# Kernel tuning notes

Measured on AMD Instinct MI355X. Metric: run time of the kernel, lower is better.

Reference implementation:

```python
import jax, jax.numpy as jnp
import numpy as np

B, H, W, C = 32, 64, 64, 192
WS, SS, NH = 8, 4, 6
N = WS * WS            # tokens per window = 64
n1, n2 = H // WS, W // WS
nW = n1 * n2           # windows per image = 64
Dh = C // NH           # head dim = 32
SCALE = Dh ** -0.5


def _rel_pos_index():
    coords = np.stack(np.meshgrid(np.arange(WS), np.arange(WS), indexing='ij')).reshape(2, -1)
    rel = (coords[:, :, None] - coords[:, None, :]).transpose(1, 2, 0)
    rel[:, :, 0] += WS - 1
    rel[:, :, 1] += WS - 1
    rel[:, :, 0] *= 2 * WS - 1
    return rel.sum(-1)  # (N, N) int


def _attn_mask():
    img = np.zeros((H, W))
    slices = (slice(0, -WS), slice(-WS, -SS), slice(-SS, None))
    cnt = 0
    for hs in slices:
        for ws in slices:
            img[hs, ws] = cnt
            cnt += 1
    mw = img.reshape(n1, WS, n2, WS).transpose(0, 2, 1, 3).reshape(nW, N)
    am = mw[:, None, :] - mw[:, :, None]  # (nW, N, N)
    return np.where(am != 0, -100.0, 0.0).astype(np.float32)


RPI = jnp.asarray(_rel_pos_index().reshape(-1))  # (N*N,) constant index
MASK = jnp.asarray(_attn_mask())                  # (nW, N, N) constant


def setup_inputs() -> dict:
    key = jax.random.key(0)
    ks = jax.random.split(key, 6)
    r = lambda k, s: jax.random.normal(k, s, jnp.float32) * 0.02
    return {
        'x': jax.random.normal(ks[0], (B, H * W, C), jnp.float32),
        'norm1_g': jnp.ones((C,), jnp.float32), 'norm1_b': jnp.zeros((C,), jnp.float32),
        'qkv_w': r(ks[1], (C, 3 * C)), 'qkv_b': jnp.zeros((3 * C,), jnp.float32),
        'proj_w': r(ks[2], (C, C)), 'proj_b': jnp.zeros((C,), jnp.float32),
        'rpb': r(ks[3], ((2 * WS - 1) ** 2, NH)),
        'norm2_g': jnp.ones((C,), jnp.float32), 'norm2_b': jnp.zeros((C,), jnp.float32),
        'fc1_w': r(ks[4], (C, 4 * C)), 'fc1_b': jnp.zeros((4 * C,), jnp.float32),
        'fc2_w': r(ks[5], (4 * C, C)), 'fc2_b': jnp.zeros((C,), jnp.float32),
    }


def _ln(x, g, b):
    m = jnp.mean(x, axis=-1, keepdims=True)
    v = jnp.mean(jnp.square(x - m), axis=-1, keepdims=True)
    return (x - m) * jax.lax.rsqrt(v + 1e-5) * g + b


def reference(x, norm1_g, norm1_b, qkv_w, qkv_b, proj_w, proj_b, rpb,
              norm2_g, norm2_b, fc1_w, fc1_b, fc2_w, fc2_b):
    shortcut = x
    h = _ln(x, norm1_g, norm1_b).reshape(B, H, W, C)
    h = jnp.roll(h, (-SS, -SS), axis=(1, 2))  # cyclic shift
    # window partition: (B, H, W, C) -> (B*nW, N, C), batch-major window order
    h = h.reshape(B, n1, WS, n2, WS, C).transpose(0, 1, 3, 2, 4, 5).reshape(B * nW, N, C)
    qkv = (h @ qkv_w + qkv_b).reshape(B * nW, N, 3, NH, Dh)
    q = qkv[:, :, 0].transpose(0, 2, 1, 3)  # (Bw, NH, N, Dh)
    k = qkv[:, :, 1].transpose(0, 2, 1, 3)
    v = qkv[:, :, 2].transpose(0, 2, 1, 3)
    scores = jnp.einsum('bhid,bhjd->bhij', q, k) * SCALE
    bias = rpb[RPI].reshape(N, N, NH).transpose(2, 0, 1)  # (NH, N, N)
    scores = scores + bias[None]
    # faithful to source: flat window axis reinterpreted as (num_w, B) for masking
    scores = (scores.reshape(nW, B, NH, N, N) + MASK[:, None, None]).reshape(B * nW, NH, N, N)
    probs = jax.nn.softmax(scores, axis=-1)
    ctx = jnp.einsum('bhij,bhjd->bhid', probs, v).transpose(0, 2, 1, 3).reshape(B * nW, N, C)
    ctx = ctx @ proj_w + proj_b
    # window reverse + un-shift
    h = ctx.reshape(B, n1, n2, WS, WS, C).transpose(0, 1, 3, 2, 4, 5).reshape(B, H, W, C)
    h = jnp.roll(h, (SS, SS), axis=(1, 2)).reshape(B, H * W, C)
    x = shortcut + h
    y = _ln(x, norm2_g, norm2_b)
    y = jax.nn.gelu(y @ fc1_w + fc1_b, approximate=False)
    return x + (y @ fc2_w + fc2_b)
```

## Files before the change

### kernel.cpp

```cpp
#include <hip/hip_runtime.h>
#include <hip/hip_bf16.h>


#define DI __device__ __forceinline__

typedef __attribute__((ext_vector_type(8))) short bhalf8;
typedef __attribute__((ext_vector_type(4))) float f32x4;
typedef unsigned short u16;
typedef unsigned int   u32;

DI u32 f2bf2(float a, float b){
  u32 r;
  asm("v_cvt_pk_bf16_f32 %0, %1, %2" : "=v"(r) : "v"(a), "v"(b));
  return r;
}
DI u16 f2bf(float f){ return (u16)f2bf2(f, f); }

DI float fast_gelu(float x){
  float s = __expf(-1.702f * x);
  return x * __builtin_amdgcn_rcpf(1.0f + s);
}

DI int tok2glob(int t){
  int n = t & 63, widx = t >> 6;
  int b = widx >> 6, wi = widx & 63;
  int hh = ((wi >> 3) << 3) + (n >> 3);
  int ww = ((wi & 7) << 3) + (n & 7);
  int hs = (hh + 4) & 63, wsv = (ww + 4) & 63;
  return (b << 12) + (hs << 6) + wsv;
}

DI int region_id(int hpos, int wpos){
  int rh = (hpos < 56) ? 0 : ((hpos < 60) ? 1 : 2);
  int rw = (wpos < 56) ? 0 : ((wpos < 60) ? 1 : 2);
  return rh*3 + rw;
}

__global__ void transcast_kernel(const float* __restrict__ W, u16* __restrict__ Wt, int K, int N){
  int idx = blockIdx.x * 256 + threadIdx.x;
  if (idx < K*N){
    int n = idx / K, k = idx - n*K;
    Wt[idx] = f2bf(W[(size_t)k * N + n]);
  }
}

__global__ __launch_bounds__(768, 3) void attn_fused_kernel(
    const float* __restrict__ x, const float* __restrict__ n1g, const float* __restrict__ n1b,
    const u16* __restrict__ qkvWt, const float* __restrict__ qkv_b,
    const u16* __restrict__ projWt, const float* __restrict__ proj_b,
    float* __restrict__ out, const float* __restrict__ rpb){
  __shared__ u16 AsB[64*192];
  __shared__ u16 QKB[64*384];
  __shared__ u16 Vt[6][32*64];
  __shared__ float Rlds[225*6];
  int widx = blockIdx.x;
  int tid  = threadIdx.x;
  int w = tid >> 6, lane = tid & 63, lr = lane & 15, lg = lane >> 4;

  if (w >= 8){
    for (int i = tid - 512; i < 225*6; i += 256) Rlds[i] = rpb[i];
  } else {
    int qrow = tid >> 3, oct = tid & 7;
    int g = tok2glob(widx*64 + qrow);
    const float4* xr = (const float4*)(x + (size_t)g*192 + oct*24);
    float4 va[6];
    float s = 0.f, sq = 0.f;
    #pragma unroll
    for (int j = 0; j < 6; j++){
      va[j] = xr[j];
      s  += va[j].x + va[j].y + va[j].z + va[j].w;
      sq += va[j].x*va[j].x + va[j].y*va[j].y + va[j].z*va[j].z + va[j].w*va[j].w;
    }
    s  += __shfl_xor(s, 1, 64);  sq += __shfl_xor(sq, 1, 64);
    s  += __shfl_xor(s, 2, 64);  sq += __shfl_xor(sq, 2, 64);
    s  += __shfl_xor(s, 4, 64);  sq += __shfl_xor(sq, 4, 64);
    float mean = s * (1.f/192.f);
    float rstd = rsqrtf(sq * (1.f/192.f) - mean*mean + 1e-5f);
    const float4* g4 = (const float4*)(n1g + oct*24);
    const float4* b4 = (const float4*)(n1b + oct*24);
    #pragma unroll
    for (int j2 = 0; j2 < 3; j2++){
      float4 v0 = va[2*j2], v1 = va[2*j2+1];
      float4 g0 = g4[2*j2], g1 = g4[2*j2+1];
      float4 b0 = b4[2*j2], b1 = b4[2*j2+1];
      uint4 pk;
      pk.x = f2bf2((v0.x-mean)*rstd*g0.x+b0.x, (v0.y-mean)*rstd*g0.y+b0.y);
      pk.y = f2bf2((v0.z-mean)*rstd*g0.z+b0.z, (v0.w-mean)*rstd*g0.w+b0.w);
      pk.z = f2bf2((v1.x-mean)*rstd*g1.x+b1.x, (v1.y-mean)*rstd*g1.y+b1.y);
      pk.w = f2bf2((v1.z-mean)*rstd*g1.z+b1.z, (v1.w-mean)*rstd*g1.w+b1.w);
      int gk = oct*3 + j2;
      *(uint4*)&AsB[qrow*192 + ((gk ^ (qrow & 7)) << 3)] = pk;
    }
  }
  __syncthreads();

  #pragma unroll
  for (int nf = 0; nf < 3; nf++){
    int cBase = w*48 + nf*16;
    bhalf8 wF[6];
    #pragma unroll
    for (int kk = 0; kk < 6; kk++)
      wF[kk] = *(const bhalf8*)&qkvWt[(size_t)(cBase + lr)*192 + kk*32 + (lg<<3)];
    float4 bv = *(const float4*)&qkv_b[cBase + (lg<<2)];
    #pragma unroll
    for (int i = 0; i < 4; i++){
      f32x4 a0 = (f32x4){0.f,0.f,0.f,0.f}, a1 = (f32x4){0.f,0.f,0.f,0.f};
      #pragma unroll
      for (int kk = 0; kk < 3; kk++){
        int row = i*16 + lr;
        bhalf8 t0 = *(const bhalf8*)&AsB[row*192 + (((2*kk*4     + lg) ^ (row & 7)) << 3)];
        bhalf8 t1 = *(const bhalf8*)&AsB[row*192 + ((((2*kk+1)*4 + lg) ^ (row & 7)) << 3)];
        a0 = __builtin_amdgcn_mfma_f32_16x16x32_bf16(wF[2*kk],   t0, a0, 0, 0, 0);
        a1 = __builtin_amdgcn_mfma_f32_16x16x32_bf16(wF[2*kk+1], t1, a1, 0, 0, 0);
      }
      float v0 = a0[0]+a1[0]+bv.x, v1 = a0[1]+a1[1]+bv.y;
      float v2 = a0[2]+a1[2]+bv.z, v3 = a0[3]+a1[3]+bv.w;
      int token = i*16 + lr;
      if (cBase < 384){
        int gq = (cBase >> 3) + (lg >> 1);
        uint2 pk; pk.x = f2bf2(v0, v1); pk.y = f2bf2(v2, v3);
        *(uint2*)&QKB[token*384 + ((gq ^ (token & 7)) << 3) + ((lg & 1) << 2)] = pk;
      } else {
        int d0 = cBase + (lg<<2) - 384;
        int hv = d0 >> 5;
        int db = d0 & 31;
        Vt[hv][(db+0)*64 + (token ^ (((db+0)&7)<<3))] = f2bf(v0);
        Vt[hv][(db+1)*64 + (token ^ (((db+1)&7)<<3))] = f2bf(v1);
        Vt[hv][(db+2)*64 + (token ^ (((db+2)&7)<<3))] = f2bf(v2);
        Vt[hv][(db+3)*64 + (token ^ (((db+3)&7)<<3))] = f2bf(v3);
      }
    }
  }
  __syncthreads();

  int hd   = (w < 6) ? w : (w - 6);
  int half = (w < 6) ? 0 : 1;
  bhalf8 qf[2], kf[4];
  #pragma unroll
  for (int i = 0; i < 2; i++){
    int token = (half*2 + i)*16 + lr;
    int gq = hd*4 + lg;
    qf[i] = *(const bhalf8*)&QKB[token*384 + ((gq ^ (token & 7)) << 3)];
  }
  #pragma unroll
  for (int j = 0; j < 4; j++){
    int token = j*16 + lr;
    int gk = 24 + hd*4 + lg;
    kf[j] = *(const bhalf8*)&QKB[token*384 + ((gk ^ (token & 7)) << 3)];
  }
  f32x4 sc[2][4];
  f32x4 zero = (f32x4){0.f,0.f,0.f,0.f};
  #pragma unroll
  for (int i = 0; i < 2; i++)
    #pragma unroll
    for (int j = 0; j < 4; j++)
      sc[i][j] = __builtin_amdgcn_mfma_f32_16x16x32_bf16(qf[i], kf[j], zero, 0, 0, 0);
  __syncthreads();

  u16* Plds = &QKB[0];
  int mwin = widx >> 5;
  int mh0 = (mwin >> 3) << 3, mw0 = (mwin & 7) << 3;
  #pragma unroll
  for (int i = 0; i < 2; i++){
    #pragma unroll
    for (int r = 0; r < 4; r++){
      int row = (half*2 + i)*16 + lg*4 + r;
      int ih = row >> 3, iw = row & 7;
      int ridr = region_id(mh0 + ih, mw0 + iw);
      float vals[4];
      #pragma unroll
      for (int j = 0; j < 4; j++){
        int col = j*16 + lr;
        int jh = col >> 3, jw = col & 7;
        float bias = Rlds[((ih-jh+7)*15 + (iw-jw+7))*6 + hd];
        int ridc = region_id(mh0 + jh, mw0 + jw);
        vals[j] = sc[i][j][r] * 0.17677669529663687f + bias + ((ridr==ridc) ? 0.f : -100.f);
      }
      float mx = fmaxf(fmaxf(vals[0],vals[1]), fmaxf(vals[2],vals[3]));
      #pragma unroll
      for (int d = 1; d < 16; d <<= 1) mx = fmaxf(mx, __shfl_xor(mx, d, 64));
      float sum = 0.f;
      #pragma unroll
      for (int j = 0; j < 4; j++){ vals[j] = __expf(vals[j]-mx); sum += vals[j]; }
      #pragma unroll
      for (int d = 1; d < 16; d <<= 1) sum += __shfl_xor(sum, d, 64);
      float inv = __builtin_amdgcn_rcpf(sum);
      #pragma unroll
      for (int j = 0; j < 4; j++){
        int col = j*16 + lr;
        Plds[hd*4096 + row*64 + (col ^ ((row & 7) << 3))] = f2bf(vals[j]*inv);
      }
    }
  }

  f32x4 oa[2][2];
  #pragma unroll
  for (int i=0;i<2;i++)
    #pragma unroll
    for (int n=0;n<2;n++) oa[i][n] = zero;
  #pragma unroll
  for (int kb = 0; kb < 2; kb++){
    bhalf8 pf[2], vf[2];
    int k = (kb<<5) + (lg<<3);
    #pragma unroll
    for (int i = 0; i < 2; i++){
      int row = (half*2 + i)*16 + lr;
      pf[i] = *(const bhalf8*)&Plds[hd*4096 + row*64 + (k ^ ((row&7)<<3))];
    }
    #pragma unroll
    for (int n = 0; n < 2; n++){
      int d = n*16 + lr;
      vf[n] = *(const bhalf8*)&Vt[hd][d*64 + (k ^ ((d&7)<<3))];
    }
    #pragma unroll
    for (int i=0;i<2;i++)
      #pragma unroll
      for (int n=0;n<2;n++)
        oa[i][n] = __builtin_amdgcn_mfma_f32_16x16x32_bf16(pf[i], vf[n], oa[i][n], 0, 0, 0);
  }

  u16* Clds = &AsB[0];
  #pragma unroll
  for (int i=0;i<2;i++)
    #pragma unroll
    for (int n=0;n<2;n++)
      #pragma unroll
      for (int r=0;r<4;r++){
        int row = (half*2 + i)*16 + lg*4 + r;
        int col = hd*32 + n*16 + lr;
        Clds[row*192 + (((col>>3) ^ (row&7)) << 3) + (col & 7)] = f2bf(oa[i][n][r]);
      }
  __syncthreads();

  f32x4 pacc[2][2];
  #pragma unroll
  for (int i=0;i<2;i++)
    #pragma unroll
    for (int n=0;n<2;n++) pacc[i][n] = zero;
  #pragma unroll
  for (int kk = 0; kk < 6; kk++){
    bhalf8 af[2], bf[2];
    #pragma unroll
    for (int i = 0; i < 2; i++){
      int row = half*32 + i*16 + lr;
      af[i] = *(const bhalf8*)&Clds[row*192 + (((kk*4 + lg) ^ (row & 7)) << 3)];
    }
    #pragma unroll
    for (int n = 0; n < 2; n++){
      int col = hd*32 + n*16 + lr;
      bf[n] = *(const bhalf8*)&projWt[(size_t)col*192 + kk*32 + (lg<<3)];
    }
    #pragma unroll
    for (int i=0;i<2;i++)
      #pragma unroll
      for (int n=0;n<2;n++)
        pacc[i][n] = __builtin_amdgcn_mfma_f32_16x16x32_bf16(af[i], bf[n], pacc[i][n], 0, 0, 0);
  }
  #pragma unroll
  for (int i=0;i<2;i++)
    #pragma unroll
    for (int n=0;n<2;n++){
      int col = hd*32 + n*16 + lr;
      float bv = proj_b[col];
      #pragma unroll
      for (int r=0;r<4;r++){
        int rowl = half*32 + i*16 + lg*4 + r;
        int g = tok2glob(widx*64 + rowl);
        size_t o = (size_t)g*192 + col;
        out[o] = x[o] + bv + pacc[i][n][r];
      }
    }
}

__global__ __launch_bounds__(256) void ln2_kernel(const float* __restrict__ X,
    const float* __restrict__ gam, const float* __restrict__ bet, u16* __restrict__ A2){
  int tid = threadIdx.x;
  int row = (blockIdx.x << 6) + (tid >> 2), quarter = tid & 3;
  const float4* xr = (const float4*)(X + (size_t)row*192 + quarter*48);
  float4 va[12];
  float s = 0.f, sq = 0.f;
  #pragma unroll
  for (int j = 0; j < 12; j++){
    va[j] = xr[j];
    s  += va[j].x + va[j].y + va[j].z + va[j].w;
    sq += va[j].x*va[j].x + va[j].y*va[j].y + va[j].z*va[j].z + va[j].w*va[j].w;
  }
  s  += __shfl_xor(s, 1, 64);  sq += __shfl_xor(sq, 1, 64);
  s  += __shfl_xor(s, 2, 64);  sq += __shfl_xor(sq, 2, 64);
  float mean = s * (1.f/192.f);
  float rstd = rsqrtf(sq * (1.f/192.f) - mean*mean + 1e-5f);
  const float4* g4 = (const float4*)(gam + quarter*48);
  const float4* b4 = (const float4*)(bet + quarter*48);
  #pragma unroll
  for (int j2 = 0; j2 < 6; j2++){
    float4 v0 = va[2*j2], v1 = va[2*j2+1];
    float4 g0 = g4[2*j2], g1 = g4[2*j2+1];
    float4 b0 = b4[2*j2], b1 = b4[2*j2+1];
    uint4 pk;
    pk.x = f2bf2((v0.x-mean)*rstd*g0.x+b0.x, (v0.y-mean)*rstd*g0.y+b0.y);
    pk.y = f2bf2((v0.z-mean)*rstd*g0.z+b0.z, (v0.w-mean)*rstd*g0.w+b0.w);
    pk.z = f2bf2((v1.x-mean)*rstd*g1.x+b1.x, (v1.y-mean)*rstd*g1.y+b1.y);
    pk.w = f2bf2((v1.z-mean)*rstd*g1.z+b1.z, (v1.w-mean)*rstd*g1.w+b1.w);
    *(uint4*)&A2[(size_t)row*192 + quarter*48 + j2*8] = pk;
  }
}

__global__ __launch_bounds__(512, 4) void fc1_kernel(const u16* __restrict__ A2,
    const u16* __restrict__ Bt, const float* __restrict__ bias, u16* __restrict__ H1){
  __shared__ u16 Wl[2][64*192];
  int tid = threadIdx.x;
  int mBase = blockIdx.x << 8;
  int lane = tid & 63, w = tid >> 6;
  int lr = lane & 15, lg = lane >> 4;
  int tokBase = mBase + (w << 5);

  bhalf8 tF[2][6];
  #pragma unroll
  for (int i = 0; i < 2; i++)
    #pragma unroll
    for (int kk = 0; kk < 6; kk++)
      tF[i][kk] = *(const bhalf8*)&A2[(size_t)(tokBase + i*16 + lr)*192 + kk*32 + (lg<<3)];

  int scol = tid >> 3, sg0 = (tid & 7) * 3;
  #define STAGE_FC1(nt, buf) { \
    const u16* sp = Bt + (size_t)((nt)*64 + scol)*192 + sg0*8; \
    _Pragma("unroll") \
    for (int j = 0; j < 3; j++){ \
      uint4 v = *(const uint4*)(sp + j*8); \
      *(uint4*)&Wl[buf][scol*192 + (((sg0 + j) ^ (scol & 7)) << 3)] = v; \
    } }

  STAGE_FC1(0, 0)
  for (int nt = 0; nt < 12; nt++){
    __syncthreads();
    if (nt < 11) STAGE_FC1(nt + 1, (nt + 1) & 1)
    int buf = nt & 1;
    #pragma unroll
    for (int cf = 0; cf < 4; cf++){
      bhalf8 wF[6];
      int col = cf*16 + lr;
      #pragma unroll
      for (int kk = 0; kk < 6; kk++)
        wF[kk] = *(const bhalf8*)&Wl[buf][col*192 + (((kk*4 + lg) ^ (col & 7)) << 3)];
      int gcol = (nt << 6) + cf*16;
      float4 bv = *(const float4*)&bias[gcol + (lg<<2)];
      #pragma unroll
      for (int i = 0; i < 2; i++){
        f32x4 a0 = (f32x4){0.f,0.f,0.f,0.f}, a1 = (f32x4){0.f,0.f,0.f,0.f};
        #pragma unroll
        for (int kk = 0; kk < 3; kk++){
          a0 = __builtin_amdgcn_mfma_f32_16x16x32_bf16(wF[2*kk],   tF[i][2*kk],   a0, 0, 0, 0);
          a1 = __builtin_amdgcn_mfma_f32_16x16x32_bf16(wF[2*kk+1], tF[i][2*kk+1], a1, 0, 0, 0);
        }
        float v0 = fast_gelu(a0[0]+a1[0]+bv.x);
        float v1 = fast_gelu(a0[1]+a1[1]+bv.y);
        float v2 = fast_gelu(a0[2]+a1[2]+bv.z);
        float v3 = fast_gelu(a0[3]+a1[3]+bv.w);
        uint2 pk; pk.x = f2bf2(v0, v1); pk.y = f2bf2(v2, v3);
        *(uint2*)&H1[(size_t)(tokBase + i*16 + lr)*768 + gcol + (lg<<2)] = pk;
      }
    }
  }
  #undef STAGE_FC1
}

__global__ __launch_bounds__(512, 2) void fc2_kernel(const u16* __restrict__ H1,
    const u16* __restrict__ Bt, const float* __restrict__ bias, float* out){
  __shared__ u16 Hl[2][256*64];
  __shared__ u16 Wl[2][192*64];
  int tid = threadIdx.x;
  int mBase = blockIdx.x << 8;
  int lane = tid & 63, w = tid >> 6;
  int lr = lane & 15, lg = lane >> 4;
  int mq = w >> 1, nh = w & 1;

  int srow = tid >> 3, sgk = tid & 7;
  #define STAGE_FC2(p, buf) { \
    _Pragma("unroll") \
    for (int j = 0; j < 4; j++){ \
      int tok = j*64 + srow; \
      uint4 v = *(const uint4*)&H1[(size_t)(mBase + tok)*768 + (p)*64 + sgk*8]; \
      *(uint4*)&Hl[buf][tok*64 + ((sgk ^ (tok & 7)) << 3)] = v; \
    } \
    _Pragma("unroll") \
    for (int j = 0; j < 3; j++){ \
      int col = j*64 + srow; \
      uint4 v = *(const uint4*)&Bt[(size_t)col*768 + (p)*64 + sgk*8]; \
      *(uint4*)&Wl[buf][col*64 + ((sgk ^ (col & 7)) << 3)] = v; \
    } }

  f32x4 acc[4][6];
  #pragma unroll
  for (int i = 0; i < 4; i++)
    #pragma unroll
    for (int cf = 0; cf < 6; cf++) acc[i][cf] = (f32x4){0.f,0.f,0.f,0.f};

  STAGE_FC2(0, 0)
  for (int p = 0; p < 12; p++){
    __syncthreads();
    if (p < 11) STAGE_FC2(p + 1, (p + 1) & 1)
    int buf = p & 1;
    #pragma unroll
    for (int kk = 0; kk < 2; kk++){
      bhalf8 hF[4], wv[6];
      #pragma unroll
      for (int i = 0; i < 4; i++){
        int tok = mq*64 + i*16 + lr;
        hF[i] = *(const bhalf8*)&Hl[buf][tok*64 + (((kk*4 + lg) ^ (tok & 7)) << 3)];
      }
      #pragma unroll
      for (int cf = 0; cf < 6; cf++){
        int col = nh*96 + cf*16 + lr;
        wv[cf] = *(const bhalf8*)&Wl[buf][col*64 + (((kk*4 + lg) ^ (col & 7)) << 3)];
      }
      #pragma unroll
      for (int i = 0; i < 4; i++)
        #pragma unroll
        for (int cf = 0; cf < 6; cf++)
          acc[i][cf] = __builtin_amdgcn_mfma_f32_16x16x32_bf16(wv[cf], hF[i], acc[i][cf], 0, 0, 0);
    }
  }
  #undef STAGE_FC2

  #pragma unroll
  for (int i = 0; i < 4; i++)
    #pragma unroll
    for (int cf = 0; cf < 6; cf++){
      int col = nh*96 + cf*16 + (lg<<2);
      float4 bv = *(const float4*)&bias[col];
      int row = mBase + mq*64 + i*16 + lr;
      float4* op = (float4*)&out[(size_t)row*192 + col];
      float4 o = *op;
      o.x += bv.x + acc[i][cf][0];
      o.y += bv.y + acc[i][cf][1];
      o.z += bv.z + acc[i][cf][2];
      o.w += bv.w + acc[i][cf][3];
      *op = o;
    }
}

extern "C" void kernel_launch(void* const* d_in, const int* in_sizes, int n_in,
                              void* d_out, int out_size, void* d_ws, size_t ws_size,
                              hipStream_t stream){
  const float* x      = (const float*)d_in[0];
  const float* n1g    = (const float*)d_in[1];
  const float* n1b    = (const float*)d_in[2];
  const float* qkv_w  = (const float*)d_in[3];
  const float* qkv_b  = (const float*)d_in[4];
  const float* proj_w = (const float*)d_in[5];
  const float* proj_b = (const float*)d_in[6];
  const float* rpb    = (const float*)d_in[7];
  const float* n2g    = (const float*)d_in[8];
  const float* n2b    = (const float*)d_in[9];
  const float* fc1_w  = (const float*)d_in[10];
  const float* fc1_b  = (const float*)d_in[11];
  const float* fc2_w  = (const float*)d_in[12];
  const float* fc2_b  = (const float*)d_in[13];
  float* out = (float*)d_out;

  const size_t T = 131072;
  u16* A2     = (u16*)d_ws;
  u16* H1     = A2 + T*192;
  u16* qkvWt  = H1 + T*768;
  u16* projWt = qkvWt + 576*192;
  u16* fc1Wt  = projWt + 192*192;
  u16* fc2Wt  = fc1Wt + 768*192;

  transcast_kernel<<<dim3((192*576+255)/256),256,0,stream>>>(qkv_w, qkvWt, 192, 576);
  transcast_kernel<<<dim3((192*192+255)/256),256,0,stream>>>(proj_w, projWt, 192, 192);
  transcast_kernel<<<dim3((192*768+255)/256),256,0,stream>>>(fc1_w, fc1Wt, 192, 768);
  transcast_kernel<<<dim3((768*192+255)/256),256,0,stream>>>(fc2_w, fc2Wt, 768, 192);

  attn_fused_kernel<<<dim3(2048),768,0,stream>>>(x, n1g, n1b, qkvWt, qkv_b,
                                                 projWt, proj_b, out, rpb);
  ln2_kernel<<<dim3(2048),256,0,stream>>>(out, n2g, n2b, A2);
  fc1_kernel<<<dim3(512),512,0,stream>>>(A2, fc1Wt, fc1_b, H1);
  fc2_kernel<<<dim3(512),512,0,stream>>>(H1, fc2Wt, fc2_b, out);
}
```

Baseline: 409.0 us.

## Drop LDS staging in fc2, prefetch proj weights and residual, add MFMA priority

fc2 no longer stages tiles through double-buffered LDS. Each wave now loads H1 and weight fragments directly from global memory, and the block shrinks to 64 tokens across 2048 blocks to raise occupancy. In the attention kernel, projection weight fragments and residual x values are loaded into registers early so their latency overlaps with earlier compute. s_setprio is placed around the MFMA bursts. These changes remove LDS traffic and barriers but add register pressure and repeated global or L2 weight reads, because tiles are no longer shared through LDS.

```diff
diff --git a/kernel.cpp b/kernel.cpp
--- a/kernel.cpp
+++ b/kernel.cpp
@@ -150,11 +150,21 @@
   }
   f32x4 sc[2][4];
   f32x4 zero = (f32x4){0.f,0.f,0.f,0.f};
+  __builtin_amdgcn_s_setprio(1);
   #pragma unroll
   for (int i = 0; i < 2; i++)
     #pragma unroll
     for (int j = 0; j < 4; j++)
       sc[i][j] = __builtin_amdgcn_mfma_f32_16x16x32_bf16(qf[i], kf[j], zero, 0, 0, 0);
+  __builtin_amdgcn_s_setprio(0);
+
+  bhalf8 pw[6][2];
+  #pragma unroll
+  for (int kk = 0; kk < 6; kk++)
+    #pragma unroll
+    for (int n = 0; n < 2; n++)
+      pw[kk][n] = *(const bhalf8*)&projWt[(size_t)(hd*32 + n*16 + lr)*192 + kk*32 + (lg<<3)];
+
   __syncthreads();
 
   u16* Plds = &QKB[0];
@@ -212,11 +222,13 @@
       int d = n*16 + lr;
       vf[n] = *(const bhalf8*)&Vt[hd][d*64 + (k ^ ((d&7)<<3))];
     }
+    __builtin_amdgcn_s_setprio(1);
     #pragma unroll
     for (int i=0;i<2;i++)
       #pragma unroll
       for (int n=0;n<2;n++)
         oa[i][n] = __builtin_amdgcn_mfma_f32_16x16x32_bf16(pf[i], vf[n], oa[i][n], 0, 0, 0);
+    __builtin_amdgcn_s_setprio(0);
   }
 
   u16* Clds = &AsB[0];
@@ -232,6 +244,19 @@
       }
   __syncthreads();
 
+  float rx[2][2][4];
+  #pragma unroll
+  for (int i=0;i<2;i++)
+    #pragma unroll
+    for (int n=0;n<2;n++){
+      int col = hd*32 + n*16 + lr;
+      #pragma unroll
+      for (int r=0;r<4;r++){
+        int rowl = half*32 + i*16 + lg*4 + r;
+        rx[i][n][r] = x[(size_t)tok2glob(widx*64 + rowl)*192 + col];
+      }
+    }
+
   f32x4 pacc[2][2];
   #pragma unroll
   for (int i=0;i<2;i++)
@@ -239,22 +264,19 @@
     for (int n=0;n<2;n++) pacc[i][n] = zero;
   #pragma unroll
   for (int kk = 0; kk < 6; kk++){
-    bhalf8 af[2], bf[2];
+    bhalf8 af[2];
     #pragma unroll
     for (int i = 0; i < 2; i++){
       int row = half*32 + i*16 + lr;
       af[i] = *(const bhalf8*)&Clds[row*192 + (((kk*4 + lg) ^ (row & 7)) << 3)];
     }
-    #pragma unroll
-    for (int n = 0; n < 2; n++){
-      int col = hd*32 + n*16 + lr;
-      bf[n] = *(const bhalf8*)&projWt[(size_t)col*192 + kk*32 + (lg<<3)];
-    }
+    __builtin_amdgcn_s_setprio(1);
     #pragma unroll
     for (int i=0;i<2;i++)
       #pragma unroll
       for (int n=0;n<2;n++)
-        pacc[i][n] = __builtin_amdgcn_mfma_f32_16x16x32_bf16(af[i], bf[n], pacc[i][n], 0, 0, 0);
+        pacc[i][n] = __builtin_amdgcn_mfma_f32_16x16x32_bf16(af[i], pw[kk][n], pacc[i][n], 0, 0, 0);
+    __builtin_amdgcn_s_setprio(0);
   }
   #pragma unroll
   for (int i=0;i<2;i++)
@@ -266,8 +288,7 @@
       for (int r=0;r<4;r++){
         int rowl = half*32 + i*16 + lg*4 + r;
         int g = tok2glob(widx*64 + rowl);
-        size_t o = (size_t)g*192 + col;
-        out[o] = x[o] + bv + pacc[i][n][r];
+        out[(size_t)g*192 + col] = rx[i][n][r] + bv + pacc[i][n][r];
       }
     }
 }
@@ -364,71 +385,47 @@
   #undef STAGE_FC1
 }
 
-__global__ __launch_bounds__(512, 2) void fc2_kernel(const u16* __restrict__ H1,
+__global__ __launch_bounds__(256, 4) void fc2_kernel(const u16* __restrict__ H1,
     const u16* __restrict__ Bt, const float* __restrict__ bias, float* out){
-  __shared__ u16 Hl[2][256*64];
-  __shared__ u16 Wl[2][192*64];
   int tid = threadIdx.x;
-  int mBase = blockIdx.x << 8;
+  int mBase = blockIdx.x << 6;
   int lane = tid & 63, w = tid >> 6;
   int lr = lane & 15, lg = lane >> 4;
   int mq = w >> 1, nh = w & 1;
-
-  int srow = tid >> 3, sgk = tid & 7;
-  #define STAGE_FC2(p, buf) { \
-    _Pragma("unroll") \
-    for (int j = 0; j < 4; j++){ \
-      int tok = j*64 + srow; \
-      uint4 v = *(const uint4*)&H1[(size_t)(mBase + tok)*768 + (p)*64 + sgk*8]; \
-      *(uint4*)&Hl[buf][tok*64 + ((sgk ^ (tok & 7)) << 3)] = v; \
-    } \
-    _Pragma("unroll") \
-    for (int j = 0; j < 3; j++){ \
-      int col = j*64 + srow; \
-      uint4 v = *(const uint4*)&Bt[(size_t)col*768 + (p)*64 + sgk*8]; \
-      *(uint4*)&Wl[buf][col*64 + ((sgk ^ (col & 7)) << 3)] = v; \
-    } }
-
-  f32x4 acc[4][6];
-  #pragma unroll
-  for (int i = 0; i < 4; i++)
+  int tokBase = mBase + (mq << 5);
+
+  f32x4 acc[2][6];
+  #pragma unroll
+  for (int i = 0; i < 2; i++)
     #pragma unroll
     for (int cf = 0; cf < 6; cf++) acc[i][cf] = (f32x4){0.f,0.f,0.f,0.f};
 
-  STAGE_FC2(0, 0)
-  for (int p = 0; p < 12; p++){
-    __syncthreads();
-    if (p < 11) STAGE_FC2(p + 1, (p + 1) & 1)
-    int buf = p & 1;
-    #pragma unroll
-    for (int kk = 0; kk < 2; kk++){
-      bhalf8 hF[4], wv[6];
-      #pragma unroll
-      for (int i = 0; i < 4; i++){
-        int tok = mq*64 + i*16 + lr;
-        hF[i] = *(const bhalf8*)&Hl[buf][tok*64 + (((kk*4 + lg) ^ (tok & 7)) << 3)];
-      }
-      #pragma unroll
-      for (int cf = 0; cf < 6; cf++){
-        int col = nh*96 + cf*16 + lr;
-        wv[cf] = *(const bhalf8*)&Wl[buf][col*64 + (((kk*4 + lg) ^ (col & 7)) << 3)];
-      }
-      #pragma unroll
-      for (int i = 0; i < 4; i++)
-        #pragma unroll
-        for (int cf = 0; cf < 6; cf++)
-          acc[i][cf] = __builtin_amdgcn_mfma_f32_16x16x32_bf16(wv[cf], hF[i], acc[i][cf], 0, 0, 0);
-    }
-  }
-  #undef STAGE_FC2
-
-  #pragma unroll
-  for (int i = 0; i < 4; i++)
+  const u16* hBase0 = H1 + (size_t)(tokBase + lr)*768 + (lg<<3);
+  const u16* hBase1 = H1 + (size_t)(tokBase + 16 + lr)*768 + (lg<<3);
+  const u16* wBase  = Bt + (size_t)(nh*96 + lr)*768 + (lg<<3);
+
+  #pragma unroll
+  for (int kb = 0; kb < 24; kb++){
+    bhalf8 hF[2], wv[6];
+    hF[0] = *(const bhalf8*)(hBase0 + kb*32);
+    hF[1] = *(const bhalf8*)(hBase1 + kb*32);
+    #pragma unroll
+    for (int cf = 0; cf < 6; cf++)
+      wv[cf] = *(const bhalf8*)(wBase + (size_t)cf*16*768 + kb*32);
+    #pragma unroll
+    for (int i = 0; i < 2; i++)
+      #pragma unroll
+      for (int cf = 0; cf < 6; cf++)
+        acc[i][cf] = __builtin_amdgcn_mfma_f32_16x16x32_bf16(wv[cf], hF[i], acc[i][cf], 0, 0, 0);
+  }
+
+  #pragma unroll
+  for (int i = 0; i < 2; i++)
     #pragma unroll
     for (int cf = 0; cf < 6; cf++){
       int col = nh*96 + cf*16 + (lg<<2);
       float4 bv = *(const float4*)&bias[col];
-      int row = mBase + mq*64 + i*16 + lr;
+      int row = tokBase + i*16 + lr;
       float4* op = (float4*)&out[(size_t)row*192 + col];
       float4 o = *op;
       o.x += bv.x + acc[i][cf][0];
@@ -475,5 +472,5 @@
                                                  projWt, proj_b, out, rpb);
   ln2_kernel<<<dim3(2048),256,0,stream>>>(out, n2g, n2b, A2);
   fc1_kernel<<<dim3(512),512,0,stream>>>(A2, fc1Wt, fc1_b, H1);
-  fc2_kernel<<<dim3(512),512,0,stream>>>(H1, fc2Wt, fc2_b, out);
-}
+  fc2_kernel<<<dim3(2048),256,0,stream>>>(H1, fc2Wt, fc2_b, out);
+}
```

Result: slower. 534.4 us (+30.7%).
